# Optimization experiments

Measured on AMD Instinct MI355X. Metric: run time of the kernel, lower is better.

Reference implementation:

```python
import jax, jax.numpy as jnp
import numpy as np

N_NODES = 10000
N_EDGES = 320000
IN_DIM = 512
HID = 64
H0 = 8
OUT = 64
H1 = 1
NEG_SLOPE = 0.2


def gat_layer(h, src, dst, W, attn_l, attn_r, n_nodes, activation=None):
    # h: (N, F_in); W: (F_in, H*D); attn_l/attn_r: (H, D)
    H, D = attn_l.shape
    feat = (h @ W).reshape(n_nodes, H, D)            # (N, H, D)
    el = jnp.einsum('nhd,hd->nh', feat, attn_l)      # (N, H)
    er = jnp.einsum('nhd,hd->nh', feat, attn_r)      # (N, H)
    e = jax.nn.leaky_relu(el[src] + er[dst], NEG_SLOPE)  # (E, H)
    # edge softmax over incoming edges of each destination node
    m = jax.ops.segment_max(e, dst, num_segments=n_nodes)   # (N, H), -inf for isolated
    m = jnp.where(jnp.isfinite(m), m, 0.0)
    ex = jnp.exp(e - m[dst])                         # (E, H)
    s = jax.ops.segment_sum(ex, dst, num_segments=n_nodes)  # (N, H)
    alpha = ex / s[dst]                              # (E, H)
    # weighted aggregation: out[dst] += alpha * feat[src]
    out = jax.ops.segment_sum(alpha[:, :, None] * feat[src], dst,
                              num_segments=n_nodes)  # (N, H, D)
    if activation is not None:
        out = activation(out)
    return out


def setup_inputs() -> dict:
    key = jax.random.key(0)
    ks = jax.random.split(key, 9)
    h = jax.random.normal(ks[0], (N_NODES, IN_DIM), dtype=jnp.float32)
    src = jax.random.randint(ks[1], (N_EDGES,), 0, N_NODES, dtype=jnp.int32)
    dst = jax.random.randint(ks[2], (N_EDGES,), 0, N_NODES, dtype=jnp.int32)
    W1 = jax.random.normal(ks[3], (IN_DIM, H0 * HID), dtype=jnp.float32) / np.sqrt(IN_DIM)
    attn_l1 = jax.random.normal(ks[4], (H0, HID), dtype=jnp.float32) / np.sqrt(HID)
    attn_r1 = jax.random.normal(ks[5], (H0, HID), dtype=jnp.float32) / np.sqrt(HID)
    W2 = jax.random.normal(ks[6], (H0 * HID, H1 * OUT), dtype=jnp.float32) / np.sqrt(H0 * HID)
    attn_l2 = jax.random.normal(ks[7], (H1, OUT), dtype=jnp.float32) / np.sqrt(OUT)
    attn_r2 = jax.random.normal(ks[8], (H1, OUT), dtype=jnp.float32) / np.sqrt(OUT)
    return {"h": h, "src": src, "dst": dst, "W1": W1, "attn_l1": attn_l1,
            "attn_r1": attn_r1, "W2": W2, "attn_l2": attn_l2, "attn_r2": attn_r2}


def reference(h, src, dst, W1, attn_l1, attn_r1, W2, attn_l2, attn_r2):
    # layer 1: elu activation, concat heads (flatten)
    x = gat_layer(h, src, dst, W1, attn_l1, attn_r1, N_NODES, activation=jax.nn.elu)
    x = x.reshape(N_NODES, H0 * HID)
    # layer 2: no activation, mean over heads
    x = gat_layer(x, src, dst, W2, attn_l2, attn_r2, N_NODES, activation=None)
    return x.mean(axis=1)  # (N, OUT)
```

## Files before the change

### kernel.cpp

```cpp
#include <hip/hip_runtime.h>
#include <hip/hip_bf16.h>
#include <math.h>

typedef unsigned int u32;
typedef unsigned short ushort;

constexpr int N_NODES = 10000;
constexpr int N_EDGES = 320000;
constexpr float NEG_SLOPE = 0.2f;

typedef __attribute__((ext_vector_type(8))) _Float16 half8;
typedef __attribute__((ext_vector_type(4))) float f32x4;
typedef __attribute__((ext_vector_type(16))) float f32x16;

__device__ __forceinline__ float lrelu(float x) { return x > 0.f ? x : NEG_SLOPE * x; }
__device__ __forceinline__ float elu(float x)   { return x > 0.f ? x : (expf(x) - 1.f); }

__device__ __forceinline__ ushort f2h(float x) {
    _Float16 h = (_Float16)x;
    return __builtin_bit_cast(ushort, h);
}
__device__ __forceinline__ float h2f(ushort u) {
    return (float)__builtin_bit_cast(_Float16, u);
}

__device__ __forceinline__ void gload16(const void* g, void* l) {
    __builtin_amdgcn_global_load_lds(
        (__attribute__((address_space(1))) void*)g,
        (__attribute__((address_space(3))) void*)l, 16, 0, 0);
}

constexpr int NB_HIST  = (N_EDGES + 255) / 256;
constexpr int NB_SPLIT = (N_NODES * 512 / 4) / 256;
constexpr int NB_T1    = 64;
constexpr int NB_T2    = 8;
constexpr int NB_WLR2  = 2;

__global__ void prep_kernel(const float4* __restrict__ h4,
                            ushort* __restrict__ xh,
                            const float* __restrict__ W1, ushort* __restrict__ w1t,
                            const float* __restrict__ W2, ushort* __restrict__ w2t,
                            const float* __restrict__ al2, const float* __restrict__ ar2,
                            float* __restrict__ wl2, float* __restrict__ wr2,
                            const int* __restrict__ dst, int* __restrict__ counts,
                            int* __restrict__ rank) {
    __shared__ float smem[64][65];
    const int b = blockIdx.x;
    if (b < NB_HIST) {
        const int i = b * 256 + threadIdx.x;
        if (i < N_EDGES) rank[i] = atomicAdd(&counts[dst[i]], 1);
    } else if (b < NB_HIST + NB_SPLIT) {
        const int i = (b - NB_HIST) * 256 + threadIdx.x;
        const float4 v = h4[i];
        *(ushort4*)&xh[i * 4] = make_ushort4(f2h(v.x), f2h(v.y), f2h(v.z), f2h(v.w));
    } else if (b < NB_HIST + NB_SPLIT + NB_T1 + NB_T2) {
        const bool isW1 = b < NB_HIST + NB_SPLIT + NB_T1;
        const float* W = isW1 ? W1 : W2;
        ushort* wt = isW1 ? w1t : w2t;
        const int N  = isW1 ? 512 : 64;
        const int t  = isW1 ? (b - NB_HIST - NB_SPLIT) : (b - NB_HIST - NB_SPLIT - NB_T1);
        const int ti = isW1 ? (t & 7) : t;
        const int tj = isW1 ? (t >> 3) : 0;
        const int c  = threadIdx.x & 63;
        const int r0 = threadIdx.x >> 6;
#pragma unroll
        for (int p = 0; p < 16; p++) {
            const int r = p * 4 + r0;
            smem[r][c] = W[(size_t)(ti * 64 + r) * N + tj * 64 + c];
        }
        __syncthreads();
#pragma unroll
        for (int p = 0; p < 16; p++) {
            const int rr = p * 4 + r0;
            wt[(size_t)(tj * 64 + rr) * 512 + ti * 64 + c] = f2h(smem[c][rr]);
        }
    } else {
        const int k = (b - NB_HIST - NB_SPLIT - NB_T1 - NB_T2) * 256 + threadIdx.x;
        float sl = 0.f, sr = 0.f;
#pragma unroll 8
        for (int d = 0; d < 64; d++) {
            const float w = W2[(size_t)k * 64 + d];
            sl += w * al2[d];
            sr += w * ar2[d];
        }
        wl2[k] = sl;
        wr2[k] = sr;
    }
}

__global__ __launch_bounds__(256) void scan_kernel(
    const int* __restrict__ counts, int* __restrict__ offs) {
    __shared__ int wsum[4];
    const int tid = threadIdx.x;
    const int lane = tid & 63, wave = tid >> 6;
    const int base = tid * 40;
    int v[40];
    int s = 0;
#pragma unroll
    for (int i = 0; i < 40; i++) {
        v[i] = (base + i < N_NODES) ? counts[base + i] : 0;
        s += v[i];
    }
    int ps = s;
#pragma unroll
    for (int o = 1; o < 64; o <<= 1) {
        const int t = __shfl_up(ps, o);
        if (lane >= o) ps += t;
    }
    if (lane == 63) wsum[wave] = ps;
    __syncthreads();
    if (tid < 4) {
        int t = wsum[tid];
#pragma unroll
        for (int o = 1; o < 4; o <<= 1) {
            const int u = __shfl_up(t, o);
            if (tid >= o) t += u;
        }
        wsum[tid] = t;
    }
    __syncthreads();
    const int wbase = (wave > 0) ? wsum[wave - 1] : 0;
    int run = wbase + ps - s;
#pragma unroll
    for (int i = 0; i < 40; i++) {
        if (base + i < N_NODES) offs[base + i + 1] = run + v[i];
        run += v[i];
    }
    if (tid == 0) offs[0] = 0;
}

constexpr int NB_GEMM1 = ((N_NODES + 63) / 64) * 4;
constexpr int NB_SCAT  = (N_EDGES + 255) / 256;

__global__ __launch_bounds__(256) void gemm1_scatter_kernel(
    const ushort* __restrict__ A, const ushort* __restrict__ B,
    ushort* __restrict__ Cout, int M,
    const float* __restrict__ attn_l, const float* __restrict__ attn_r,
    float* __restrict__ elp, float* __restrict__ erp,
    const int* __restrict__ src, const int* __restrict__ dst,
    const int* __restrict__ rank, const int* __restrict__ offs,
    int* __restrict__ srcs) {
    constexpr int BM = 64, BN = 128, BK = 32, K = 512, N = 512;

    if ((int)blockIdx.x >= NB_GEMM1) {
        const int i = ((int)blockIdx.x - NB_GEMM1) * 256 + threadIdx.x;
        if (i < N_EDGES) srcs[offs[dst[i]] + rank[i]] = src[i];
        return;
    }

    __shared__ __align__(16) ushort sA[BM * BK];
    __shared__ __align__(16) ushort sB[BN * BK];

    const int tid = threadIdx.x;
    const int wave = tid >> 6, lane = tid & 63;
    const int m0 = ((int)blockIdx.x >> 2) * BM, n0 = ((int)blockIdx.x & 3) * BN;
    const int wm = wave >> 1, wn = wave & 1;
    const int l31 = lane & 31, lh = lane >> 5;

    const int fb = wave * 1024 + lane * 16;

    int arow = m0 + (fb >> 6);
    if (arow > M - 1) arow = M - 1;
    const size_t abyte = (size_t)arow * (K * 2) + (fb & 63);
    size_t bbyte[2];
#pragma unroll
    for (int r = 0; r < 2; r++) {
        const int f = fb + r * 4096;
        bbyte[r] = (size_t)(n0 + (f >> 6)) * (K * 2) + (f & 63);
    }

    f32x16 acc[2] = {};

    for (int k0 = 0; k0 < K; k0 += BK) {
        __syncthreads();
        const size_t kb = (size_t)k0 * 2;
        gload16((const char*)A + abyte + kb, (char*)sA + fb);
#pragma unroll
        for (int r = 0; r < 2; r++) {
            const int f = fb + r * 4096;
            gload16((const char*)B + bbyte[r] + kb, (char*)sB + f);
        }
        __syncthreads();

#pragma unroll
        for (int ks = 0; ks < 2; ks++) {
            const int koff = ks * 16 + lh * 8;
            const half8 ah = *(const half8*)&sA[(wm * 32 + l31) * BK + koff];
#pragma unroll
            for (int ni = 0; ni < 2; ni++) {
                const half8 bh = *(const half8*)&sB[(wn * 64 + ni * 32 + l31) * BK + koff];
                acc[ni] = __builtin_amdgcn_mfma_f32_32x32x16_f16(ah, bh, acc[ni], 0, 0, 0);
            }
        }
    }

#pragma unroll
    for (int reg = 0; reg < 16; reg++) {
        const int grow = m0 + wm * 32 + (reg & 3) + 8 * (reg >> 2) + 4 * lh;
        if (grow < M) {
#pragma unroll
            for (int ni = 0; ni < 2; ni++) {
                const int gcol = n0 + wn * 64 + ni * 32 + l31;
                Cout[(size_t)grow * N + gcol] = f2h(acc[ni][reg]);
            }
        }
    }

    const int head = (n0 + wn * 64) >> 6;
    float alv[2], arv[2];
#pragma unroll
    for (int ni = 0; ni < 2; ni++) {
        alv[ni] = attn_l[head * 64 + ni * 32 + l31];
        arv[ni] = attn_r[head * 64 + ni * 32 + l31];
    }
#pragma unroll
    for (int reg = 0; reg < 16; reg++) {
        float pl = acc[0][reg] * alv[0] + acc[1][reg] * alv[1];
        float pr = acc[0][reg] * arv[0] + acc[1][reg] * arv[1];
#pragma unroll
        for (int o = 1; o < 32; o <<= 1) {
            pl += __shfl_xor(pl, o);
            pr += __shfl_xor(pr, o);
        }
        const int grow = m0 + wm * 32 + (reg & 3) + 8 * (reg >> 2) + 4 * lh;
        if (l31 == 0 && grow < M) {
            elp[grow * 8 + head] = pl;
            erp[grow * 8 + head] = pr;
        }
    }
}

__global__ __launch_bounds__(256) void agg1_kernel(
    const ushort* __restrict__ feat, const float* __restrict__ el,
    const float* __restrict__ er, const int* __restrict__ offs,
    const int* __restrict__ srcs, ushort* __restrict__ xh,
    const float* __restrict__ wl2, const float* __restrict__ wr2,
    float* __restrict__ el2, float* __restrict__ er2) {
    const int tid = threadIdx.x;
    const int wave = tid >> 6, lane = tid & 63;
    const int node = blockIdx.x * 4 + wave;
    const int start = offs[node];
    const int deg = offs[node + 1] - start;
    const int d0 = lane * 8;
    const int myh = lane >> 3;

    if (deg == 0) {
        const ushort4 z = make_ushort4(0, 0, 0, 0);
        *(ushort4*)&xh[(size_t)node * 512 + d0] = z;
        *(ushort4*)&xh[(size_t)node * 512 + d0 + 4] = z;
        if (lane == 0) { el2[node] = 0.f; er2[node] = 0.f; }
        return;
    }

    const float4 ea = *(const float4*)&er[node * 8];
    const float4 eb = *(const float4*)&er[node * 8 + 4];
    const float er_my = (myh & 4) ? ((myh & 2) ? ((myh & 1) ? eb.w : eb.z)
                                              : ((myh & 1) ? eb.y : eb.x))
                                  : ((myh & 2) ? ((myh & 1) ? ea.w : ea.z)
                                              : ((myh & 1) ? ea.y : ea.x));

    float acc[8];
#pragma unroll
    for (int i = 0; i < 8; i++) acc[i] = 0.f;
    float ws = 0.f;

    for (int base = 0; base < deg; base += 64) {
        const int has = min(64, deg - base);
        const int s = srcs[start + base + min(lane, has - 1)];
        int j = 0;

        float eqA[8]; half8 uqA[8];
        if (j + 8 <= has) {
            int sqA[8];
#pragma unroll
            for (int q = 0; q < 8; q++) sqA[q] = __shfl(s, q);
#pragma unroll
            for (int q = 0; q < 8; q++) eqA[q] = el[sqA[q] * 8 + myh];
#pragma unroll
            for (int q = 0; q < 8; q++)
                uqA[q] = *(const half8*)&feat[(size_t)sqA[q] * 512 + d0];
        }
        for (; j + 16 <= has; j += 8) {
            int sqB[8]; float eqB[8]; half8 uqB[8];
#pragma unroll
            for (int q = 0; q < 8; q++) sqB[q] = __shfl(s, j + 8 + q);
#pragma unroll
            for (int q = 0; q < 8; q++) eqB[q] = el[sqB[q] * 8 + myh];
#pragma unroll
            for (int q = 0; q < 8; q++)
                uqB[q] = *(const half8*)&feat[(size_t)sqB[q] * 512 + d0];
            float wq[8];
#pragma unroll
            for (int q = 0; q < 8; q++) wq[q] = __expf(lrelu(eqA[q] + er_my));
#pragma unroll
            for (int q = 0; q < 8; q++) {
#pragma unroll
                for (int i = 0; i < 8; i++)
                    acc[i] += wq[q] * (float)uqA[q][i];
                ws += wq[q];
            }
#pragma unroll
            for (int q = 0; q < 8; q++) { eqA[q] = eqB[q]; uqA[q] = uqB[q]; }
        }
        if (j + 8 <= has) {
            float wq[8];
#pragma unroll
            for (int q = 0; q < 8; q++) wq[q] = __expf(lrelu(eqA[q] + er_my));
#pragma unroll
            for (int q = 0; q < 8; q++) {
#pragma unroll
                for (int i = 0; i < 8; i++)
                    acc[i] += wq[q] * (float)uqA[q][i];
                ws += wq[q];
            }
            j += 8;
        }
        for (; j < has; j++) {
            const int sj = __shfl(s, j);
            const float w = __expf(lrelu(el[sj * 8 + myh] + er_my));
            const half8 u = *(const half8*)&feat[(size_t)sj * 512 + d0];
#pragma unroll
            for (int i = 0; i < 8; i++)
                acc[i] += w * (float)u[i];
            ws += w;
        }
    }

    const float inv = 1.f / ws;
    float o[8];
#pragma unroll
    for (int i = 0; i < 8; i++) o[i] = elu(acc[i] * inv);

    const float4 wla = *(const float4*)&wl2[d0];
    const float4 wlb = *(const float4*)&wl2[d0 + 4];
    const float4 wra = *(const float4*)&wr2[d0];
    const float4 wrb = *(const float4*)&wr2[d0 + 4];
    float pl = o[0] * wla.x + o[1] * wla.y + o[2] * wla.z + o[3] * wla.w
             + o[4] * wlb.x + o[5] * wlb.y + o[6] * wlb.z + o[7] * wlb.w;
    float pr = o[0] * wra.x + o[1] * wra.y + o[2] * wra.z + o[3] * wra.w
             + o[4] * wrb.x + o[5] * wrb.y + o[6] * wrb.z + o[7] * wrb.w;
#pragma unroll
    for (int off = 32; off > 0; off >>= 1) {
        pl += __shfl_xor(pl, off);
        pr += __shfl_xor(pr, off);
    }
    if (lane == 0) { el2[node] = pl; er2[node] = pr; }

    ushort hh[8];
#pragma unroll
    for (int i = 0; i < 8; i++) hh[i] = f2h(o[i]);
    *(ushort4*)&xh[(size_t)node * 512 + d0]     = make_ushort4(hh[0], hh[1], hh[2], hh[3]);
    *(ushort4*)&xh[(size_t)node * 512 + d0 + 4] = make_ushort4(hh[4], hh[5], hh[6], hh[7]);
}

__global__ __launch_bounds__(256) void gemm2_kernel(
    const ushort* __restrict__ A, const ushort* __restrict__ B,
    ushort* __restrict__ Cout, int M) {
    constexpr int BM = 64, BN = 64, BK = 32, K = 512, N = 64;
    constexpr int WM = 32, WN = 32, MT_M = 2, MT_N = 2;

    __shared__ __align__(16) ushort sA[BM * BK];
    __shared__ __align__(16) ushort sB[BN * BK];

    const int tid = threadIdx.x;
    const int wave = tid >> 6, lane = tid & 63;
    const int m0 = blockIdx.x * BM;
    const int wm = wave >> 1, wn = wave & 1;
    const int quad = lane >> 4, l15 = lane & 15;

    const int fb = wave * 1024 + lane * 16;

    int arow = m0 + (fb >> 6);
    if (arow > M - 1) arow = M - 1;
    const size_t abyte = (size_t)arow * (K * 2) + (fb & 63);
    const size_t bbyte = (size_t)(fb >> 6) * (K * 2) + (fb & 63);

    f32x4 acc[MT_M][MT_N] = {};

    for (int k0 = 0; k0 < K; k0 += BK) {
        __syncthreads();
        const size_t kb = (size_t)k0 * 2;
        gload16((const char*)A + abyte + kb, (char*)sA + fb);
        gload16((const char*)B + bbyte + kb, (char*)sB + fb);
        __syncthreads();

        half8 ah[MT_M], bh[MT_N];
#pragma unroll
        for (int mi = 0; mi < MT_M; mi++) {
            const int row = wm * WM + mi * 16 + l15;
            ah[mi] = *(const half8*)&sA[row * BK + quad * 8];
        }
#pragma unroll
        for (int ni = 0; ni < MT_N; ni++) {
            const int row = wn * WN + ni * 16 + l15;
            bh[ni] = *(const half8*)&sB[row * BK + quad * 8];
        }
#pragma unroll
        for (int mi = 0; mi < MT_M; mi++)
#pragma unroll
            for (int ni = 0; ni < MT_N; ni++)
                acc[mi][ni] = __builtin_amdgcn_mfma_f32_16x16x32_f16(ah[mi], bh[ni], acc[mi][ni], 0, 0, 0);
    }

#pragma unroll
    for (int mi = 0; mi < MT_M; mi++) {
#pragma unroll
        for (int r = 0; r < 4; r++) {
            const int grow = m0 + wm * WM + mi * 16 + quad * 4 + r;
            if (grow < M) {
#pragma unroll
                for (int ni = 0; ni < MT_N; ni++) {
                    const int gcol = wn * WN + ni * 16 + l15;
                    Cout[(size_t)grow * N + gcol] = f2h(acc[mi][ni][r]);
                }
            }
        }
    }
}

__global__ __launch_bounds__(256) void agg2_kernel(
    const ushort* __restrict__ feat, const float* __restrict__ el,
    const float* __restrict__ er, const int* __restrict__ offs,
    const int* __restrict__ srcs, float* __restrict__ out) {
    const int tid = threadIdx.x;
    const int wave = tid >> 6, lane = tid & 63;
    const int node = blockIdx.x * 4 + wave;
    const int start = offs[node];
    const int deg = offs[node + 1] - start;
    if (deg == 0) { out[(size_t)node * 64 + lane] = 0.f; return; }
    const float ern = er[node];

    float acc = 0.f, ws = 0.f;
    for (int base = 0; base < deg; base += 64) {
        const int has = min(64, deg - base);
        const int s = srcs[start + base + min(lane, has - 1)];
        const float w = __expf(lrelu(el[s] + ern));
        int j = 0;
        for (; j + 8 <= has; j += 8) {
            float aq[8]; int sq[8];
#pragma unroll
            for (int q = 0; q < 8; q++) { aq[q] = __shfl(w, j + q); sq[q] = __shfl(s, j + q); }
            ushort fq[8];
#pragma unroll
            for (int q = 0; q < 8; q++) fq[q] = feat[(size_t)sq[q] * 64 + lane];
#pragma unroll
            for (int q = 0; q < 8; q++) { acc += aq[q] * h2f(fq[q]); ws += aq[q]; }
        }
        for (; j < has; j++) {
            const float a = __shfl(w, j);
            const int sj = __shfl(s, j);
            acc += a * h2f(feat[(size_t)sj * 64 + lane]);
            ws += a;
        }
    }
    out[(size_t)node * 64 + lane] = acc / ws;
}

extern "C" void kernel_launch(void* const* d_in, const int* in_sizes, int n_in,
                              void* d_out, int out_size, void* d_ws, size_t ws_size,
                              hipStream_t stream) {
    const float* h   = (const float*)d_in[0];
    const int*   src = (const int*)d_in[1];
    const int*   dst = (const int*)d_in[2];
    const float* W1  = (const float*)d_in[3];
    const float* al1 = (const float*)d_in[4];
    const float* ar1 = (const float*)d_in[5];
    const float* W2  = (const float*)d_in[6];
    const float* al2 = (const float*)d_in[7];
    const float* ar2 = (const float*)d_in[8];
    float* out = (float*)d_out;

    char* p = (char*)d_ws;
    ushort* feat1 = (ushort*)p; p += (size_t)N_NODES * 512 * 2;
    ushort* feat2 = (ushort*)p; p += (size_t)N_NODES * 64 * 2;
    float* el1   = (float*)p;  p += (size_t)N_NODES * 8 * 4;
    float* er1   = (float*)p;  p += (size_t)N_NODES * 8 * 4;
    float* el2   = (float*)p;  p += (size_t)N_NODES * 4;
    float* er2   = (float*)p;  p += (size_t)N_NODES * 4;
    ushort* xh   = (ushort*)p; p += (size_t)N_NODES * 512 * 2;
    ushort* w1t  = (ushort*)p; p += (size_t)512 * 512 * 2;
    ushort* w2t  = (ushort*)p; p += (size_t)64 * 512 * 2;
    float* wl2   = (float*)p;  p += (size_t)512 * 4;
    float* wr2   = (float*)p;  p += (size_t)512 * 4;
    int* counts  = (int*)p;    p += (size_t)N_NODES * 4;
    int* offs    = (int*)p;    p += (size_t)10004 * 4;
    int* rank    = (int*)p;    p += (size_t)N_EDGES * 4;
    int* srcs    = (int*)p;    p += (size_t)N_EDGES * 4;

    hipMemsetAsync(counts, 0, (size_t)N_NODES * 4, stream);

    prep_kernel<<<NB_HIST + NB_SPLIT + NB_T1 + NB_T2 + NB_WLR2, 256, 0, stream>>>(
        (const float4*)h, xh, W1, w1t, W2, w2t, al2, ar2, wl2, wr2,
        dst, counts, rank);

    scan_kernel<<<1, 256, 0, stream>>>(counts, offs);

    gemm1_scatter_kernel<<<NB_GEMM1 + NB_SCAT, 256, 0, stream>>>(
        xh, w1t, feat1, N_NODES, al1, ar1, el1, er1,
        src, dst, rank, offs, srcs);

    agg1_kernel<<<N_NODES / 4, 256, 0, stream>>>(
        feat1, el1, er1, offs, srcs, xh, wl2, wr2, el2, er2);

    gemm2_kernel<<<(N_NODES + 63) / 64, 256, 0, stream>>>(
        xh, w2t, feat2, N_NODES);

    agg2_kernel<<<N_NODES / 4, 256, 0, stream>>>(feat2, el2, er2, offs, srcs, out);
}
```

Before: 194.6 us.

## Use persistent waves with atomic node work queue in aggregation kernels

Both aggregation kernels now launch a fixed grid of 512 blocks in which each wave repeatedly pulls the next destination node from a global atomic counter, replacing the one-wave-per-node static launch. This aims to balance work across varying in-degrees and to avoid the cost of launching and retiring many short blocks. The software-pipelined prefetch of the next 8 edges in agg1 is removed, so memory latency depends more on occupancy. Each node now pays a serialized atomic, and the counters are zeroed by widening the existing memset.

New measurement: 433.7 us. +122.9%, slower.

```diff
diff --git a/kernel.cpp b/kernel.cpp
--- a/kernel.cpp
+++ b/kernel.cpp
@@ -235,122 +235,102 @@
     const float* __restrict__ er, const int* __restrict__ offs,
     const int* __restrict__ srcs, ushort* __restrict__ xh,
     const float* __restrict__ wl2, const float* __restrict__ wr2,
-    float* __restrict__ el2, float* __restrict__ er2) {
+    float* __restrict__ el2, float* __restrict__ er2,
+    int* __restrict__ wq) {
     const int tid = threadIdx.x;
-    const int wave = tid >> 6, lane = tid & 63;
-    const int node = blockIdx.x * 4 + wave;
-    const int start = offs[node];
-    const int deg = offs[node + 1] - start;
+    const int lane = tid & 63;
     const int d0 = lane * 8;
     const int myh = lane >> 3;
 
-    if (deg == 0) {
-        const ushort4 z = make_ushort4(0, 0, 0, 0);
-        *(ushort4*)&xh[(size_t)node * 512 + d0] = z;
-        *(ushort4*)&xh[(size_t)node * 512 + d0 + 4] = z;
-        if (lane == 0) { el2[node] = 0.f; er2[node] = 0.f; }
-        return;
-    }
-
-    const float4 ea = *(const float4*)&er[node * 8];
-    const float4 eb = *(const float4*)&er[node * 8 + 4];
-    const float er_my = (myh & 4) ? ((myh & 2) ? ((myh & 1) ? eb.w : eb.z)
-                                              : ((myh & 1) ? eb.y : eb.x))
-                                  : ((myh & 2) ? ((myh & 1) ? ea.w : ea.z)
-                                              : ((myh & 1) ? ea.y : ea.x));
-
-    float acc[8];
-#pragma unroll
-    for (int i = 0; i < 8; i++) acc[i] = 0.f;
-    float ws = 0.f;
-
-    for (int base = 0; base < deg; base += 64) {
-        const int has = min(64, deg - base);
-        const int s = srcs[start + base + min(lane, has - 1)];
-        int j = 0;
-
-        float eqA[8]; half8 uqA[8];
-        if (j + 8 <= has) {
-            int sqA[8];
-#pragma unroll
-            for (int q = 0; q < 8; q++) sqA[q] = __shfl(s, q);
-#pragma unroll
-            for (int q = 0; q < 8; q++) eqA[q] = el[sqA[q] * 8 + myh];
-#pragma unroll
-            for (int q = 0; q < 8; q++)
-                uqA[q] = *(const half8*)&feat[(size_t)sqA[q] * 512 + d0];
-        }
-        for (; j + 16 <= has; j += 8) {
-            int sqB[8]; float eqB[8]; half8 uqB[8];
-#pragma unroll
-            for (int q = 0; q < 8; q++) sqB[q] = __shfl(s, j + 8 + q);
-#pragma unroll
-            for (int q = 0; q < 8; q++) eqB[q] = el[sqB[q] * 8 + myh];
-#pragma unroll
-            for (int q = 0; q < 8; q++)
-                uqB[q] = *(const half8*)&feat[(size_t)sqB[q] * 512 + d0];
-            float wq[8];
-#pragma unroll
-            for (int q = 0; q < 8; q++) wq[q] = __expf(lrelu(eqA[q] + er_my));
-#pragma unroll
-            for (int q = 0; q < 8; q++) {
-#pragma unroll
-                for (int i = 0; i < 8; i++)
-                    acc[i] += wq[q] * (float)uqA[q][i];
-                ws += wq[q];
+    int node;
+    if (lane == 0) node = atomicAdd(wq, 1);
+    node = __shfl(node, 0);
+
+    while (node < N_NODES) {
+        const int start = offs[node];
+        const int deg = offs[node + 1] - start;
+
+        float o[8];
+#pragma unroll
+        for (int i = 0; i < 8; i++) o[i] = 0.f;
+
+        if (deg > 0) {
+            const float4 ea = *(const float4*)&er[node * 8];
+            const float4 eb = *(const float4*)&er[node * 8 + 4];
+            const float er_my = (myh & 4) ? ((myh & 2) ? ((myh & 1) ? eb.w : eb.z)
+                                                      : ((myh & 1) ? eb.y : eb.x))
+                                          : ((myh & 2) ? ((myh & 1) ? ea.w : ea.z)
+                                                      : ((myh & 1) ? ea.y : ea.x));
+            float acc[8];
+#pragma unroll
+            for (int i = 0; i < 8; i++) acc[i] = 0.f;
+            float ws = 0.f;
+
+            for (int base = 0; base < deg; base += 64) {
+                const int has = min(64, deg - base);
+                const int s = srcs[start + base + min(lane, has - 1)];
+                int j = 0;
+                for (; j + 8 <= has; j += 8) {
+                    int sq[8];
+#pragma unroll
+                    for (int q = 0; q < 8; q++) sq[q] = __shfl(s, j + q);
+                    float eq[8];
+#pragma unroll
+                    for (int q = 0; q < 8; q++) eq[q] = el[sq[q] * 8 + myh];
+                    half8 uq[8];
+#pragma unroll
+                    for (int q = 0; q < 8; q++)
+                        uq[q] = *(const half8*)&feat[(size_t)sq[q] * 512 + d0];
+                    float wqv[8];
+#pragma unroll
+                    for (int q = 0; q < 8; q++) wqv[q] = __expf(lrelu(eq[q] + er_my));
+#pragma unroll
+                    for (int q = 0; q < 8; q++) {
+#pragma unroll
+                        for (int i = 0; i < 8; i++)
+                            acc[i] += wqv[q] * (float)uq[q][i];
+                        ws += wqv[q];
+                    }
+                }
+                for (; j < has; j++) {
+                    const int sj = __shfl(s, j);
+                    const float w = __expf(lrelu(el[sj * 8 + myh] + er_my));
+                    const half8 u = *(const half8*)&feat[(size_t)sj * 512 + d0];
+#pragma unroll
+                    for (int i = 0; i < 8; i++)
+                        acc[i] += w * (float)u[i];
+                    ws += w;
+                }
             }
-#pragma unroll
-            for (int q = 0; q < 8; q++) { eqA[q] = eqB[q]; uqA[q] = uqB[q]; }
-        }
-        if (j + 8 <= has) {
-            float wq[8];
-#pragma unroll
-            for (int q = 0; q < 8; q++) wq[q] = __expf(lrelu(eqA[q] + er_my));
-#pragma unroll
-            for (int q = 0; q < 8; q++) {
-#pragma unroll
-                for (int i = 0; i < 8; i++)
-                    acc[i] += wq[q] * (float)uqA[q][i];
-                ws += wq[q];
-            }
-            j += 8;
-        }
-        for (; j < has; j++) {
-            const int sj = __shfl(s, j);
-            const float w = __expf(lrelu(el[sj * 8 + myh] + er_my));
-            const half8 u = *(const half8*)&feat[(size_t)sj * 512 + d0];
-#pragma unroll
-            for (int i = 0; i < 8; i++)
-                acc[i] += w * (float)u[i];
-            ws += w;
-        }
-    }
-
-    const float inv = 1.f / ws;
-    float o[8];
-#pragma unroll
-    for (int i = 0; i < 8; i++) o[i] = elu(acc[i] * inv);
-
-    const float4 wla = *(const float4*)&wl2[d0];
-    const float4 wlb = *(const float4*)&wl2[d0 + 4];
-    const float4 wra = *(const float4*)&wr2[d0];
-    const float4 wrb = *(const float4*)&wr2[d0 + 4];
-    float pl = o[0] * wla.x + o[1] * wla.y + o[2] * wla.z + o[3] * wla.w
-             + o[4] * wlb.x + o[5] * wlb.y + o[6] * wlb.z + o[7] * wlb.w;
-    float pr = o[0] * wra.x + o[1] * wra.y + o[2] * wra.z + o[3] * wra.w
-             + o[4] * wrb.x + o[5] * wrb.y + o[6] * wrb.z + o[7] * wrb.w;
-#pragma unroll
-    for (int off = 32; off > 0; off >>= 1) {
-        pl += __shfl_xor(pl, off);
-        pr += __shfl_xor(pr, off);
-    }
-    if (lane == 0) { el2[node] = pl; er2[node] = pr; }
-
-    ushort hh[8];
-#pragma unroll
-    for (int i = 0; i < 8; i++) hh[i] = f2h(o[i]);
-    *(ushort4*)&xh[(size_t)node * 512 + d0]     = make_ushort4(hh[0], hh[1], hh[2], hh[3]);
-    *(ushort4*)&xh[(size_t)node * 512 + d0 + 4] = make_ushort4(hh[4], hh[5], hh[6], hh[7]);
+            const float inv = 1.f / ws;
+#pragma unroll
+            for (int i = 0; i < 8; i++) o[i] = elu(acc[i] * inv);
+        }
+
+        const float4 wla = *(const float4*)&wl2[d0];
+        const float4 wlb = *(const float4*)&wl2[d0 + 4];
+        const float4 wra = *(const float4*)&wr2[d0];
+        const float4 wrb = *(const float4*)&wr2[d0 + 4];
+        float pl = o[0] * wla.x + o[1] * wla.y + o[2] * wla.z + o[3] * wla.w
+                 + o[4] * wlb.x + o[5] * wlb.y + o[6] * wlb.z + o[7] * wlb.w;
+        float pr = o[0] * wra.x + o[1] * wra.y + o[2] * wra.z + o[3] * wra.w
+                 + o[4] * wrb.x + o[5] * wrb.y + o[6] * wrb.z + o[7] * wrb.w;
+#pragma unroll
+        for (int off = 32; off > 0; off >>= 1) {
+            pl += __shfl_xor(pl, off);
+            pr += __shfl_xor(pr, off);
+        }
+        if (lane == 0) { el2[node] = pl; er2[node] = pr; }
+
+        ushort hh[8];
+#pragma unroll
+        for (int i = 0; i < 8; i++) hh[i] = f2h(o[i]);
+        *(ushort4*)&xh[(size_t)node * 512 + d0]     = make_ushort4(hh[0], hh[1], hh[2], hh[3]);
+        *(ushort4*)&xh[(size_t)node * 512 + d0 + 4] = make_ushort4(hh[4], hh[5], hh[6], hh[7]);
+
+        if (lane == 0) node = atomicAdd(wq, 1);
+        node = __shfl(node, 0);
+    }
 }
 
 __global__ __launch_bounds__(256) void gemm2_kernel(
@@ -421,39 +401,50 @@
 __global__ __launch_bounds__(256) void agg2_kernel(
     const ushort* __restrict__ feat, const float* __restrict__ el,
     const float* __restrict__ er, const int* __restrict__ offs,
-    const int* __restrict__ srcs, float* __restrict__ out) {
+    const int* __restrict__ srcs, float* __restrict__ out,
+    int* __restrict__ wq) {
     const int tid = threadIdx.x;
-    const int wave = tid >> 6, lane = tid & 63;
-    const int node = blockIdx.x * 4 + wave;
-    const int start = offs[node];
-    const int deg = offs[node + 1] - start;
-    if (deg == 0) { out[(size_t)node * 64 + lane] = 0.f; return; }
-    const float ern = er[node];
-
-    float acc = 0.f, ws = 0.f;
-    for (int base = 0; base < deg; base += 64) {
-        const int has = min(64, deg - base);
-        const int s = srcs[start + base + min(lane, has - 1)];
-        const float w = __expf(lrelu(el[s] + ern));
-        int j = 0;
-        for (; j + 8 <= has; j += 8) {
-            float aq[8]; int sq[8];
-#pragma unroll
-            for (int q = 0; q < 8; q++) { aq[q] = __shfl(w, j + q); sq[q] = __shfl(s, j + q); }
-            ushort fq[8];
-#pragma unroll
-            for (int q = 0; q < 8; q++) fq[q] = feat[(size_t)sq[q] * 64 + lane];
-#pragma unroll
-            for (int q = 0; q < 8; q++) { acc += aq[q] * h2f(fq[q]); ws += aq[q]; }
-        }
-        for (; j < has; j++) {
-            const float a = __shfl(w, j);
-            const int sj = __shfl(s, j);
-            acc += a * h2f(feat[(size_t)sj * 64 + lane]);
-            ws += a;
-        }
-    }
-    out[(size_t)node * 64 + lane] = acc / ws;
+    const int lane = tid & 63;
+
+    int node;
+    if (lane == 0) node = atomicAdd(wq, 1);
+    node = __shfl(node, 0);
+
+    while (node < N_NODES) {
+        const int start = offs[node];
+        const int deg = offs[node + 1] - start;
+        if (deg == 0) {
+            out[(size_t)node * 64 + lane] = 0.f;
+        } else {
+            const float ern = er[node];
+            float acc = 0.f, ws = 0.f;
+            for (int base = 0; base < deg; base += 64) {
+                const int has = min(64, deg - base);
+                const int s = srcs[start + base + min(lane, has - 1)];
+                const float w = __expf(lrelu(el[s] + ern));
+                int j = 0;
+                for (; j + 8 <= has; j += 8) {
+                    float aq[8]; int sq[8];
+#pragma unroll
+                    for (int q = 0; q < 8; q++) { aq[q] = __shfl(w, j + q); sq[q] = __shfl(s, j + q); }
+                    ushort fq[8];
+#pragma unroll
+                    for (int q = 0; q < 8; q++) fq[q] = feat[(size_t)sq[q] * 64 + lane];
+#pragma unroll
+                    for (int q = 0; q < 8; q++) { acc += aq[q] * h2f(fq[q]); ws += aq[q]; }
+                }
+                for (; j < has; j++) {
+                    const float a = __shfl(w, j);
+                    const int sj = __shfl(s, j);
+                    acc += a * h2f(feat[(size_t)sj * 64 + lane]);
+                    ws += a;
+                }
+            }
+            out[(size_t)node * 64 + lane] = acc / ws;
+        }
+        if (lane == 0) node = atomicAdd(wq, 1);
+        node = __shfl(node, 0);
+    }
 }
 
 extern "C" void kernel_launch(void* const* d_in, const int* in_sizes, int n_in,
@@ -483,11 +474,12 @@
     float* wl2   = (float*)p;  p += (size_t)512 * 4;
     float* wr2   = (float*)p;  p += (size_t)512 * 4;
     int* counts  = (int*)p;    p += (size_t)N_NODES * 4;
+    int* wqs     = (int*)p;    p += 16;
     int* offs    = (int*)p;    p += (size_t)10004 * 4;
     int* rank    = (int*)p;    p += (size_t)N_EDGES * 4;
     int* srcs    = (int*)p;    p += (size_t)N_EDGES * 4;
 
-    hipMemsetAsync(counts, 0, (size_t)N_NODES * 4, stream);
+    hipMemsetAsync(counts, 0, (size_t)N_NODES * 4 + 16, stream);
 
     prep_kernel<<<NB_HIST + NB_SPLIT + NB_T1 + NB_T2 + NB_WLR2, 256, 0, stream>>>(
         (const float4*)h, xh, W1, w1t, W2, w2t, al2, ar2, wl2, wr2,
@@ -499,11 +491,11 @@
         xh, w1t, feat1, N_NODES, al1, ar1, el1, er1,
         src, dst, rank, offs, srcs);
 
-    agg1_kernel<<<N_NODES / 4, 256, 0, stream>>>(
-        feat1, el1, er1, offs, srcs, xh, wl2, wr2, el2, er2);
+    agg1_kernel<<<512, 256, 0, stream>>>(
+        feat1, el1, er1, offs, srcs, xh, wl2, wr2, el2, er2, &wqs[0]);
 
     gemm2_kernel<<<(N_NODES + 63) / 64, 256, 0, stream>>>(
         xh, w2t, feat2, N_NODES);
 
-    agg2_kernel<<<N_NODES / 4, 256, 0, stream>>>(feat2, el2, er2, offs, srcs, out);
-}
+    agg2_kernel<<<512, 256, 0, stream>>>(feat2, el2, er2, offs, srcs, out, &wqs[1]);
+}
```
